# Performance work log

Measured on AMD Instinct MI355X. Metric: run time of the kernel, lower is better.

The kernel has to match this reference:

```python
import jax, jax.numpy as jnp
import numpy as np

TOP_K = 2

def setup_inputs() -> dict:
    key = jax.random.key(0)
    k1, k2, k3, k4, k5 = jax.random.split(key, 5)
    T, H, I, E = 2048, 2048, 2048, 8
    scale = 0.02
    return {
        "hidden_states": jax.random.normal(k1, (T, H), dtype=jnp.float32),
        "gate_w": jax.random.normal(k2, (E, H), dtype=jnp.float32) * scale,  # router Linear weight [E, H]
        "w1": jax.random.normal(k3, (E, H, I), dtype=jnp.float32) * scale,   # gate proj per expert
        "w3": jax.random.normal(k4, (E, H, I), dtype=jnp.float32) * scale,   # up proj per expert
        "w2": jax.random.normal(k5, (E, I, H), dtype=jnp.float32) * scale,   # down proj per expert
    }

def reference(hidden_states, gate_w, w1, w3, w2):
    T, H = hidden_states.shape
    E = gate_w.shape[0]
    # Router gate in float32 (ReplicatedLinear with params_dtype=float32, no bias)
    router_logits = jnp.einsum('th,eh->te', hidden_states.astype(jnp.float32), gate_w)
    probs = jax.nn.softmax(router_logits, axis=-1)  # [T, E]
    topk_w, topk_idx = jax.lax.top_k(probs, TOP_K)   # [T, K]
    topk_w = topk_w / jnp.sum(topk_w, axis=-1, keepdims=True)  # renormalize=True
    # Dense combine weights: zero for non-selected experts
    rows = jnp.arange(T)[:, None]
    comb = jnp.zeros((T, E), dtype=hidden_states.dtype).at[rows, topk_idx].add(
        topk_w.astype(hidden_states.dtype))
    # SwiGLU experts computed densely per expert, masked-combined
    g = jnp.einsum('th,ehi->tei', hidden_states, w1)   # gate proj
    u = jnp.einsum('th,ehi->tei', hidden_states, w3)   # up proj
    act = jax.nn.silu(g) * u                            # [T, E, I]
    y = jnp.einsum('tei,eih->teh', act, w2)             # down proj [T, E, H]
    out = jnp.einsum('te,teh->th', comb, y)             # weighted combine
    return out
```

## Files before the change

### kernel.cpp

```cpp
#include <hip/hip_runtime.h>
#include <hip/hip_bf16.h>

#define T_TOK 2048
#define H_DIM 2048
#define I_DIM 2048
#define E_NUM 8
#define TOPK  2

#define BM 128
#define BN 128
#define BK 64

typedef float  floatx4 __attribute__((ext_vector_type(4)));
typedef __bf16 bf16x8  __attribute__((ext_vector_type(8)));
typedef __bf16 bf16x4  __attribute__((ext_vector_type(4)));

__device__ __forceinline__ int swz(int row, int g) {
    return (row * 8 + (g ^ ((row >> 1) & 7))) * 16;
}

__global__ __launch_bounds__(64) void router_kernel(
    const float* __restrict__ hs, const float* __restrict__ gate_w,
    int* __restrict__ counts, int* __restrict__ lists, float* __restrict__ wpair)
{
    const int t    = blockIdx.x;
    const int lane = threadIdx.x;

    float acc[E_NUM];
#pragma unroll
    for (int e = 0; e < E_NUM; e++) acc[e] = 0.f;

    const float4* hsrow = (const float4*)(hs + (size_t)t * H_DIM);
#pragma unroll
    for (int it = 0; it < (H_DIM / 4) / 64; it++) {
        const int c = lane + it * 64;
        const float4 x = hsrow[c];
#pragma unroll
        for (int e = 0; e < E_NUM; e++) {
            const float4 w = ((const float4*)(gate_w + (size_t)e * H_DIM))[c];
            acc[e] += x.x * w.x + x.y * w.y + x.z * w.z + x.w * w.w;
        }
    }
#pragma unroll
    for (int e = 0; e < E_NUM; e++) {
        float v = acc[e];
        for (int off = 32; off >= 1; off >>= 1) v += __shfl_xor(v, off, 64);
        acc[e] = v;
    }
    if (lane == 0) {
        float l0 = -1e30f; int i0 = 0;
        for (int e = 0; e < E_NUM; e++) if (acc[e] > l0) { l0 = acc[e]; i0 = e; }
        float l1 = -1e30f; int i1 = (i0 == 0) ? 1 : 0;
        for (int e = 0; e < E_NUM; e++) if (e != i0 && acc[e] > l1) { l1 = acc[e]; i1 = e; }
        const float e1 = __expf(l1 - l0);
        const float s  = 1.f + e1;
        const int p0 = atomicAdd(&counts[i0], 1);
        lists[i0 * T_TOK + p0] = 2 * t;
        const int p1 = atomicAdd(&counts[i1], 1);
        lists[i1 * T_TOK + p1] = 2 * t + 1;
        wpair[2 * t]     = 1.f / s;
        wpair[2 * t + 1] = e1 / s;
    }
}

__global__ __launch_bounds__(256, 2) void gemm1_kernel(
    const float* __restrict__ hs, const float* __restrict__ w1,
    const float* __restrict__ w3, const int* __restrict__ counts,
    const int* __restrict__ lists, __bf16* __restrict__ Abuf)
{
    const int e   = blockIdx.z;
    const int n_e = counts[e];
    const int m0  = blockIdx.y * BM;
    if (m0 >= n_e) return;
    const int n0 = blockIdx.x * BN;

    const int*   list = lists + e * T_TOK;
    const float* w1e  = w1 + (size_t)e * H_DIM * I_DIM;
    const float* w3e  = w3 + (size_t)e * H_DIM * I_DIM;

    __shared__ __align__(16) __bf16 Xs [BM * BK];
    __shared__ __align__(16) __bf16 B1s[BN * BK];
    __shared__ __align__(16) __bf16 B3s[BN * BK];

    const int tid = threadIdx.x;
    const int xm = tid >> 4;
    const int xg = (tid & 15) >> 1;
    const int xh = tid & 1;
    const int kb = tid >> 5;
    const int nc = tid & 31;

    int tok[8];
#pragma unroll
    for (int i = 0; i < 8; i++) {
        const int r = m0 + xm + 16 * i;
        tok[i] = (r < n_e) ? (list[r] >> 1) : 0;
    }

    const int wave = tid >> 6;
    const int lane = tid & 63;
    const int wm   = (wave >> 1) * 64;
    const int wn   = (wave & 1) * 64;
    const int lrow = lane & 15;
    const int quad = lane >> 4;

    floatx4 accG[4][4], accU[4][4];
#pragma unroll
    for (int i = 0; i < 4; i++)
#pragma unroll
        for (int j = 0; j < 4; j++) {
            accG[i][j] = (floatx4){0.f, 0.f, 0.f, 0.f};
            accU[i][j] = (floatx4){0.f, 0.f, 0.f, 0.f};
        }

    for (int k0 = 0; k0 < H_DIM; k0 += BK) {
#pragma unroll
        for (int i = 0; i < 8; i++) {
            const int m = xm + 16 * i;
            const float4 x = *(const float4*)(hs + (size_t)tok[i] * H_DIM + k0 + xg * 8 + xh * 4);
            const bf16x4 v = {(__bf16)x.x, (__bf16)x.y, (__bf16)x.z, (__bf16)x.w};
            *(bf16x4*)((char*)Xs + swz(m, xg) + xh * 8) = v;
        }
        {
            float4 f[8];
#pragma unroll
            for (int j = 0; j < 8; j++)
                f[j] = *(const float4*)(w1e + (size_t)(k0 + 8 * kb + j) * I_DIM + n0 + 4 * nc);
#pragma unroll
            for (int nn = 0; nn < 4; nn++) {
                bf16x8 w;
#pragma unroll
                for (int j = 0; j < 8; j++) w[j] = (__bf16)((const float*)&f[j])[nn];
                *(bf16x8*)((char*)B1s + swz(4 * nc + nn, kb)) = w;
            }
        }
        {
            float4 f[8];
#pragma unroll
            for (int j = 0; j < 8; j++)
                f[j] = *(const float4*)(w3e + (size_t)(k0 + 8 * kb + j) * I_DIM + n0 + 4 * nc);
#pragma unroll
            for (int nn = 0; nn < 4; nn++) {
                bf16x8 w;
#pragma unroll
                for (int j = 0; j < 8; j++) w[j] = (__bf16)((const float*)&f[j])[nn];
                *(bf16x8*)((char*)B3s + swz(4 * nc + nn, kb)) = w;
            }
        }
        __syncthreads();

#pragma unroll
        for (int s = 0; s < 2; s++) {
            bf16x8 af[4], b1f[4], b3f[4];
#pragma unroll
            for (int i = 0; i < 4; i++)
                af[i]  = *(const bf16x8*)((char*)Xs  + swz(wm + i * 16 + lrow, 4 * s + quad));
#pragma unroll
            for (int j = 0; j < 4; j++) {
                b1f[j] = *(const bf16x8*)((char*)B1s + swz(wn + j * 16 + lrow, 4 * s + quad));
                b3f[j] = *(const bf16x8*)((char*)B3s + swz(wn + j * 16 + lrow, 4 * s + quad));
            }
#pragma unroll
            for (int i = 0; i < 4; i++)
#pragma unroll
                for (int j = 0; j < 4; j++) {
                    accG[i][j] = __builtin_amdgcn_mfma_f32_16x16x32_bf16(af[i], b1f[j], accG[i][j], 0, 0, 0);
                    accU[i][j] = __builtin_amdgcn_mfma_f32_16x16x32_bf16(af[i], b3f[j], accU[i][j], 0, 0, 0);
                }
        }
        __syncthreads();
    }

#pragma unroll
    for (int i = 0; i < 4; i++) {
#pragma unroll
        for (int r = 0; r < 4; r++) {
            const int row = m0 + wm + i * 16 + quad * 4 + r;
            if (row < n_e) {
                const int p = list[row];
                __bf16* dst = Abuf + (size_t)p * I_DIM + n0 + wn + lrow;
#pragma unroll
                for (int j = 0; j < 4; j++) {
                    const float g = accG[i][j][r];
                    const float u = accU[i][j][r];
                    const float sv = g / (1.f + __expf(-g));
                    dst[j * 16] = (__bf16)(sv * u);
                }
            }
        }
    }
}

__global__ __launch_bounds__(256, 2) void gemm2_kernel(
    const __bf16* __restrict__ Abuf, const float* __restrict__ w2,
    const int* __restrict__ counts, const int* __restrict__ lists,
    __bf16* __restrict__ Ybuf)
{
    const int e   = blockIdx.z;
    const int n_e = counts[e];
    const int m0  = blockIdx.y * BM;
    if (m0 >= n_e) return;
    const int n0 = blockIdx.x * BN;

    const int*   list = lists + e * T_TOK;
    const float* w2e  = w2 + (size_t)e * I_DIM * H_DIM;

    __shared__ __align__(16) __bf16 As[BM * BK];
    __shared__ __align__(16) __bf16 Bs[BN * BK];

    const int tid = threadIdx.x;
    const int am = tid >> 3;
    const int ag = tid & 7;
    const int kb = tid >> 5;
    const int nc = tid & 31;

    int prow[4];
#pragma unroll
    for (int i = 0; i < 4; i++) {
        const int r = m0 + am + 32 * i;
        prow[i] = (r < n_e) ? list[r] : 0;
    }

    const int wave = tid >> 6;
    const int lane = tid & 63;
    const int wm   = (wave >> 1) * 64;
    const int wn   = (wave & 1) * 64;
    const int lrow = lane & 15;
    const int quad = lane >> 4;

    floatx4 acc[4][4];
#pragma unroll
    for (int i = 0; i < 4; i++)
#pragma unroll
        for (int j = 0; j < 4; j++) acc[i][j] = (floatx4){0.f, 0.f, 0.f, 0.f};

    for (int k0 = 0; k0 < I_DIM; k0 += BK) {
#pragma unroll
        for (int i = 0; i < 4; i++) {
            const int m = am + 32 * i;
            const bf16x8 v = *(const bf16x8*)(Abuf + (size_t)prow[i] * I_DIM + k0 + 8 * ag);
            *(bf16x8*)((char*)As + swz(m, ag)) = v;
        }
        {
            float4 f[8];
#pragma unroll
            for (int j = 0; j < 8; j++)
                f[j] = *(const float4*)(w2e + (size_t)(k0 + 8 * kb + j) * H_DIM + n0 + 4 * nc);
#pragma unroll
            for (int nn = 0; nn < 4; nn++) {
                bf16x8 w;
#pragma unroll
                for (int j = 0; j < 8; j++) w[j] = (__bf16)((const float*)&f[j])[nn];
                *(bf16x8*)((char*)Bs + swz(4 * nc + nn, kb)) = w;
            }
        }
        __syncthreads();

#pragma unroll
        for (int s = 0; s < 2; s++) {
            bf16x8 af[4], bf[4];
#pragma unroll
            for (int i = 0; i < 4; i++)
                af[i] = *(const bf16x8*)((char*)As + swz(wm + i * 16 + lrow, 4 * s + quad));
#pragma unroll
            for (int j = 0; j < 4; j++)
                bf[j] = *(const bf16x8*)((char*)Bs + swz(wn + j * 16 + lrow, 4 * s + quad));
#pragma unroll
            for (int i = 0; i < 4; i++)
#pragma unroll
                for (int j = 0; j < 4; j++)
                    acc[i][j] = __builtin_amdgcn_mfma_f32_16x16x32_bf16(af[i], bf[j], acc[i][j], 0, 0, 0);
        }
        __syncthreads();
    }

#pragma unroll
    for (int i = 0; i < 4; i++) {
#pragma unroll
        for (int r = 0; r < 4; r++) {
            const int row = m0 + wm + i * 16 + quad * 4 + r;
            if (row < n_e) {
                const int p = list[row];
                __bf16* dst = Ybuf + (size_t)p * H_DIM + n0 + wn + lrow;
#pragma unroll
                for (int j = 0; j < 4; j++) dst[j * 16] = (__bf16)acc[i][j][r];
            }
        }
    }
}

__global__ __launch_bounds__(256) void combine_kernel(
    const __bf16* __restrict__ Ybuf, const float* __restrict__ wpair,
    float* __restrict__ out)
{
    const int idx = blockIdx.x * 256 + threadIdx.x;
    const int t   = idx >> 9;
    const int hc  = (idx & 511) * 4;
    const float w0 = wpair[2 * t];
    const float w1 = wpair[2 * t + 1];
    const __bf16* y0 = Ybuf + (size_t)(2 * t) * H_DIM + hc;
    const __bf16* y1 = y0 + H_DIM;
    float4 o;
    o.x = w0 * (float)y0[0] + w1 * (float)y1[0];
    o.y = w0 * (float)y0[1] + w1 * (float)y1[1];
    o.z = w0 * (float)y0[2] + w1 * (float)y1[2];
    o.w = w0 * (float)y0[3] + w1 * (float)y1[3];
    *(float4*)(out + (size_t)t * H_DIM + hc) = o;
}

extern "C" void kernel_launch(void* const* d_in, const int* in_sizes, int n_in,
                              void* d_out, int out_size, void* d_ws, size_t ws_size,
                              hipStream_t stream)
{
    const float* hs     = (const float*)d_in[0];
    const float* gate_w = (const float*)d_in[1];
    const float* w1     = (const float*)d_in[2];
    const float* w3     = (const float*)d_in[3];
    const float* w2     = (const float*)d_in[4];
    float*       out    = (float*)d_out;

    char* ws = (char*)d_ws;
    int*    counts = (int*)(ws + 0);
    float*  wpair  = (float*)(ws + 1024);
    int*    lists  = (int*)(ws + 32768);
    __bf16* Abuf   = (__bf16*)(ws + (1 << 17));
    __bf16* Ybuf   = (__bf16*)(ws + (1 << 17) +
                               (size_t)2 * T_TOK * I_DIM * sizeof(__bf16));

    hipMemsetAsync(counts, 0, E_NUM * sizeof(int), stream);

    router_kernel<<<T_TOK, 64, 0, stream>>>(hs, gate_w, counts, lists, wpair);

    gemm1_kernel<<<dim3(I_DIM / BN, T_TOK / BM, E_NUM), 256, 0, stream>>>(
        hs, w1, w3, counts, lists, Abuf);

    gemm2_kernel<<<dim3(H_DIM / BN, T_TOK / BM, E_NUM), 256, 0, stream>>>(
        Abuf, w2, counts, lists, Ybuf);

    combine_kernel<<<(T_TOK * H_DIM / 4) / 256, 256, 0, stream>>>(Ybuf, wpair, out);
}
```

Before: 728.7 us.

## Pre-convert activations to bf16 in router and shrink GEMM N-tile to 64

Measured after the change: 600.0 us. 1.21x faster.

```diff
diff --git a/kernel.cpp b/kernel.cpp
--- a/kernel.cpp
+++ b/kernel.cpp
@@ -8,7 +8,7 @@
 #define TOPK  2
 
 #define BM 128
-#define BN 128
+#define BN 64
 #define BK 64
 
 typedef float  floatx4 __attribute__((ext_vector_type(4)));
@@ -21,7 +21,8 @@
 
 __global__ __launch_bounds__(64) void router_kernel(
     const float* __restrict__ hs, const float* __restrict__ gate_w,
-    int* __restrict__ counts, int* __restrict__ lists, float* __restrict__ wpair)
+    int* __restrict__ counts, int* __restrict__ lists, float* __restrict__ wpair,
+    __bf16* __restrict__ Xbf)
 {
     const int t    = blockIdx.x;
     const int lane = threadIdx.x;
@@ -35,6 +36,8 @@
     for (int it = 0; it < (H_DIM / 4) / 64; it++) {
         const int c = lane + it * 64;
         const float4 x = hsrow[c];
+        const bf16x4 v = {(__bf16)x.x, (__bf16)x.y, (__bf16)x.z, (__bf16)x.w};
+        *(bf16x4*)(Xbf + (size_t)t * H_DIM + 4 * c) = v;
 #pragma unroll
         for (int e = 0; e < E_NUM; e++) {
             const float4 w = ((const float4*)(gate_w + (size_t)e * H_DIM))[c];
@@ -63,8 +66,8 @@
     }
 }
 
-__global__ __launch_bounds__(256, 2) void gemm1_kernel(
-    const float* __restrict__ hs, const float* __restrict__ w1,
+__global__ __launch_bounds__(256, 3) void gemm1_kernel(
+    const __bf16* __restrict__ Xbf, const float* __restrict__ w1,
     const float* __restrict__ w3, const int* __restrict__ counts,
     const int* __restrict__ lists, __bf16* __restrict__ Abuf)
 {
@@ -83,86 +86,80 @@
     __shared__ __align__(16) __bf16 B3s[BN * BK];
 
     const int tid = threadIdx.x;
-    const int xm = tid >> 4;
-    const int xg = (tid & 15) >> 1;
-    const int xh = tid & 1;
+    const int xr8 = tid >> 3;
+    const int xg  = tid & 7;
     const int kb = tid >> 5;
-    const int nc = tid & 31;
-
-    int tok[8];
-#pragma unroll
-    for (int i = 0; i < 8; i++) {
-        const int r = m0 + xm + 16 * i;
+    const int np = tid & 31;
+
+    int tok[4];
+#pragma unroll
+    for (int i = 0; i < 4; i++) {
+        const int r = m0 + xr8 + 32 * i;
         tok[i] = (r < n_e) ? (list[r] >> 1) : 0;
     }
 
     const int wave = tid >> 6;
     const int lane = tid & 63;
     const int wm   = (wave >> 1) * 64;
-    const int wn   = (wave & 1) * 64;
+    const int wn   = (wave & 1) * 32;
     const int lrow = lane & 15;
     const int quad = lane >> 4;
 
-    floatx4 accG[4][4], accU[4][4];
+    floatx4 accG[4][2], accU[4][2];
 #pragma unroll
     for (int i = 0; i < 4; i++)
 #pragma unroll
-        for (int j = 0; j < 4; j++) {
+        for (int j = 0; j < 2; j++) {
             accG[i][j] = (floatx4){0.f, 0.f, 0.f, 0.f};
             accU[i][j] = (floatx4){0.f, 0.f, 0.f, 0.f};
         }
 
     for (int k0 = 0; k0 < H_DIM; k0 += BK) {
 #pragma unroll
-        for (int i = 0; i < 8; i++) {
-            const int m = xm + 16 * i;
-            const float4 x = *(const float4*)(hs + (size_t)tok[i] * H_DIM + k0 + xg * 8 + xh * 4);
-            const bf16x4 v = {(__bf16)x.x, (__bf16)x.y, (__bf16)x.z, (__bf16)x.w};
-            *(bf16x4*)((char*)Xs + swz(m, xg) + xh * 8) = v;
+        for (int i = 0; i < 4; i++) {
+            const int m = xr8 + 32 * i;
+            const bf16x8 v = *(const bf16x8*)(Xbf + (size_t)tok[i] * H_DIM + k0 + 8 * xg);
+            *(bf16x8*)((char*)Xs + swz(m, xg)) = v;
         }
         {
-            float4 f[8];
-#pragma unroll
-            for (int j = 0; j < 8; j++)
-                f[j] = *(const float4*)(w1e + (size_t)(k0 + 8 * kb + j) * I_DIM + n0 + 4 * nc);
-#pragma unroll
-            for (int nn = 0; nn < 4; nn++) {
-                bf16x8 w;
-#pragma unroll
-                for (int j = 0; j < 8; j++) w[j] = (__bf16)((const float*)&f[j])[nn];
-                *(bf16x8*)((char*)B1s + swz(4 * nc + nn, kb)) = w;
-            }
+            const float* src = w1e + (size_t)(k0 + 8 * kb) * I_DIM + n0 + 2 * np;
+            float2 f[8];
+#pragma unroll
+            for (int j = 0; j < 8; j++) f[j] = *(const float2*)(src + (size_t)j * I_DIM);
+            bf16x8 wlo, whi;
+#pragma unroll
+            for (int j = 0; j < 8; j++) { wlo[j] = (__bf16)f[j].x; whi[j] = (__bf16)f[j].y; }
+            *(bf16x8*)((char*)B1s + swz(2 * np,     kb)) = wlo;
+            *(bf16x8*)((char*)B1s + swz(2 * np + 1, kb)) = whi;
         }
         {
-            float4 f[8];
-#pragma unroll
-            for (int j = 0; j < 8; j++)
-                f[j] = *(const float4*)(w3e + (size_t)(k0 + 8 * kb + j) * I_DIM + n0 + 4 * nc);
-#pragma unroll
-            for (int nn = 0; nn < 4; nn++) {
-                bf16x8 w;
-#pragma unroll
-                for (int j = 0; j < 8; j++) w[j] = (__bf16)((const float*)&f[j])[nn];
-                *(bf16x8*)((char*)B3s + swz(4 * nc + nn, kb)) = w;
-            }
+            const float* src = w3e + (size_t)(k0 + 8 * kb) * I_DIM + n0 + 2 * np;
+            float2 f[8];
+#pragma unroll
+            for (int j = 0; j < 8; j++) f[j] = *(const float2*)(src + (size_t)j * I_DIM);
+            bf16x8 wlo, whi;
+#pragma unroll
+            for (int j = 0; j < 8; j++) { wlo[j] = (__bf16)f[j].x; whi[j] = (__bf16)f[j].y; }
+            *(bf16x8*)((char*)B3s + swz(2 * np,     kb)) = wlo;
+            *(bf16x8*)((char*)B3s + swz(2 * np + 1, kb)) = whi;
         }
         __syncthreads();
 
 #pragma unroll
         for (int s = 0; s < 2; s++) {
-            bf16x8 af[4], b1f[4], b3f[4];
+            bf16x8 af[4], b1f[2], b3f[2];
 #pragma unroll
             for (int i = 0; i < 4; i++)
                 af[i]  = *(const bf16x8*)((char*)Xs  + swz(wm + i * 16 + lrow, 4 * s + quad));
 #pragma unroll
-            for (int j = 0; j < 4; j++) {
+            for (int j = 0; j < 2; j++) {
                 b1f[j] = *(const bf16x8*)((char*)B1s + swz(wn + j * 16 + lrow, 4 * s + quad));
                 b3f[j] = *(const bf16x8*)((char*)B3s + swz(wn + j * 16 + lrow, 4 * s + quad));
             }
 #pragma unroll
             for (int i = 0; i < 4; i++)
 #pragma unroll
-                for (int j = 0; j < 4; j++) {
+                for (int j = 0; j < 2; j++) {
                     accG[i][j] = __builtin_amdgcn_mfma_f32_16x16x32_bf16(af[i], b1f[j], accG[i][j], 0, 0, 0);
                     accU[i][j] = __builtin_amdgcn_mfma_f32_16x16x32_bf16(af[i], b3f[j], accU[i][j], 0, 0, 0);
                 }
@@ -179,7 +176,7 @@
                 const int p = list[row];
                 __bf16* dst = Abuf + (size_t)p * I_DIM + n0 + wn + lrow;
 #pragma unroll
-                for (int j = 0; j < 4; j++) {
+                for (int j = 0; j < 2; j++) {
                     const float g = accG[i][j][r];
                     const float u = accU[i][j][r];
                     const float sv = g / (1.f + __expf(-g));
@@ -190,7 +187,7 @@
     }
 }
 
-__global__ __launch_bounds__(256, 2) void gemm2_kernel(
+__global__ __launch_bounds__(256, 4) void gemm2_kernel(
     const __bf16* __restrict__ Abuf, const float* __restrict__ w2,
     const int* __restrict__ counts, const int* __restrict__ lists,
     __bf16* __restrict__ Ybuf)
@@ -208,66 +205,64 @@
     __shared__ __align__(16) __bf16 Bs[BN * BK];
 
     const int tid = threadIdx.x;
-    const int am = tid >> 3;
-    const int ag = tid & 7;
-    const int kb = tid >> 5;
-    const int nc = tid & 31;
+    const int ar8 = tid >> 3;
+    const int ag  = tid & 7;
+    const int kb  = tid >> 5;
+    const int np  = tid & 31;
 
     int prow[4];
 #pragma unroll
     for (int i = 0; i < 4; i++) {
-        const int r = m0 + am + 32 * i;
+        const int r = m0 + ar8 + 32 * i;
         prow[i] = (r < n_e) ? list[r] : 0;
     }
 
     const int wave = tid >> 6;
     const int lane = tid & 63;
     const int wm   = (wave >> 1) * 64;
-    const int wn   = (wave & 1) * 64;
+    const int wn   = (wave & 1) * 32;
     const int lrow = lane & 15;
     const int quad = lane >> 4;
 
-    floatx4 acc[4][4];
+    floatx4 acc[4][2];
 #pragma unroll
     for (int i = 0; i < 4; i++)
 #pragma unroll
-        for (int j = 0; j < 4; j++) acc[i][j] = (floatx4){0.f, 0.f, 0.f, 0.f};
+        for (int j = 0; j < 2; j++) acc[i][j] = (floatx4){0.f, 0.f, 0.f, 0.f};
 
     for (int k0 = 0; k0 < I_DIM; k0 += BK) {
 #pragma unroll
         for (int i = 0; i < 4; i++) {
-            const int m = am + 32 * i;
+            const int m = ar8 + 32 * i;
             const bf16x8 v = *(const bf16x8*)(Abuf + (size_t)prow[i] * I_DIM + k0 + 8 * ag);
             *(bf16x8*)((char*)As + swz(m, ag)) = v;
         }
         {
-            float4 f[8];
-#pragma unroll
-            for (int j = 0; j < 8; j++)
-                f[j] = *(const float4*)(w2e + (size_t)(k0 + 8 * kb + j) * H_DIM + n0 + 4 * nc);
-#pragma unroll
-            for (int nn = 0; nn < 4; nn++) {
-                bf16x8 w;
-#pragma unroll
-                for (int j = 0; j < 8; j++) w[j] = (__bf16)((const float*)&f[j])[nn];
-                *(bf16x8*)((char*)Bs + swz(4 * nc + nn, kb)) = w;
-            }
+            const float* src = w2e + (size_t)(k0 + 8 * kb) * H_DIM + n0 + 2 * np;
+            float2 f[8];
+#pragma unroll
+            for (int j = 0; j < 8; j++) f[j] = *(const float2*)(src + (size_t)j * H_DIM);
+            bf16x8 wlo, whi;
+#pragma unroll
+            for (int j = 0; j < 8; j++) { wlo[j] = (__bf16)f[j].x; whi[j] = (__bf16)f[j].y; }
+            *(bf16x8*)((char*)Bs + swz(2 * np,     kb)) = wlo;
+            *(bf16x8*)((char*)Bs + swz(2 * np + 1, kb)) = whi;
         }
         __syncthreads();
 
 #pragma unroll
         for (int s = 0; s < 2; s++) {
-            bf16x8 af[4], bf[4];
+            bf16x8 af[4], bf[2];
 #pragma unroll
             for (int i = 0; i < 4; i++)
                 af[i] = *(const bf16x8*)((char*)As + swz(wm + i * 16 + lrow, 4 * s + quad));
 #pragma unroll
-            for (int j = 0; j < 4; j++)
+            for (int j = 0; j < 2; j++)
                 bf[j] = *(const bf16x8*)((char*)Bs + swz(wn + j * 16 + lrow, 4 * s + quad));
 #pragma unroll
             for (int i = 0; i < 4; i++)
 #pragma unroll
-                for (int j = 0; j < 4; j++)
+                for (int j = 0; j < 2; j++)
                     acc[i][j] = __builtin_amdgcn_mfma_f32_16x16x32_bf16(af[i], bf[j], acc[i][j], 0, 0, 0);
         }
         __syncthreads();
@@ -282,7 +277,7 @@
                 const int p = list[row];
                 __bf16* dst = Ybuf + (size_t)p * H_DIM + n0 + wn + lrow;
 #pragma unroll
-                for (int j = 0; j < 4; j++) dst[j * 16] = (__bf16)acc[i][j][r];
+                for (int j = 0; j < 2; j++) dst[j * 16] = (__bf16)acc[i][j][r];
             }
         }
     }
@@ -322,16 +317,17 @@
     int*    counts = (int*)(ws + 0);
     float*  wpair  = (float*)(ws + 1024);
     int*    lists  = (int*)(ws + 32768);
-    __bf16* Abuf   = (__bf16*)(ws + (1 << 17));
-    __bf16* Ybuf   = (__bf16*)(ws + (1 << 17) +
-                               (size_t)2 * T_TOK * I_DIM * sizeof(__bf16));
+    __bf16* Xbf    = (__bf16*)(ws + (1 << 17));
+    __bf16* Ybuf   = (__bf16*)(ws + (1 << 17));
+    __bf16* Abuf   = (__bf16*)(ws + (1 << 17) +
+                               (size_t)2 * T_TOK * H_DIM * sizeof(__bf16));
 
     hipMemsetAsync(counts, 0, E_NUM * sizeof(int), stream);
 
-    router_kernel<<<T_TOK, 64, 0, stream>>>(hs, gate_w, counts, lists, wpair);
+    router_kernel<<<T_TOK, 64, 0, stream>>>(hs, gate_w, counts, lists, wpair, Xbf);
 
     gemm1_kernel<<<dim3(I_DIM / BN, T_TOK / BM, E_NUM), 256, 0, stream>>>(
-        hs, w1, w3, counts, lists, Abuf);
+        Xbf, w1, w3, counts, lists, Abuf);
 
     gemm2_kernel<<<dim3(H_DIM / BN, T_TOK / BM, E_NUM), 256, 0, stream>>>(
         Abuf, w2, counts, lists, Ybuf);
```
